# Optimization experiments

Measured on AMD Instinct MI355X. Metric: run time of the kernel, lower is better.

Reference implementation:

```python
import jax, jax.numpy as jnp
import numpy as np

EPS = 1e-12


def agnn_layer(x, row, col, num_nodes):
    """AGNN propagation with beta frozen at 1.0 (requires_grad=False in source).
    alpha_ij = softmax_{j in N(i)} ( beta * cos(x_i, x_j) ); out_i = sum_j alpha_ij * x_j.
    row = destination node of each edge (segment id), col = source node.
    """
    xn = x / (jnp.linalg.norm(x, axis=-1, keepdims=True) + EPS)  # unit-norm features
    score = jnp.sum(xn[row] * xn[col], axis=-1)                   # [E] beta=1 * cos sim
    smax = jax.ops.segment_max(score, row, num_segments=num_nodes)
    e = jnp.exp(score - smax[row])                                # stable softmax numerator
    denom = jax.ops.segment_sum(e, row, num_segments=num_nodes)
    alpha = e / jnp.maximum(denom[row], EPS)                      # [E]
    out = jax.ops.segment_sum(alpha[:, None] * x[col], row, num_segments=num_nodes)
    return out


def setup_inputs() -> dict:
    key = jax.random.key(0)
    ks = jax.random.split(key, 8)
    N, E = 100000, 1600000
    IN_DIM, HID, OUT_DIM = 128, 64, 64
    x = jax.random.normal(ks[0], (N, IN_DIM), dtype=jnp.float32)
    edge_row = jnp.sort(jax.random.randint(ks[1], (E,), 0, N))
    edge_col = jax.random.randint(ks[2], (E,), 0, N)
    # Linear params (PyTorch nn.Linear style: y = x @ W.T + b)
    s1 = 1.0 / np.sqrt(IN_DIM)
    W1 = jax.random.uniform(ks[3], (HID, IN_DIM), jnp.float32, -s1, s1)
    b1 = jax.random.uniform(ks[4], (HID,), jnp.float32, -s1, s1)
    s2 = 1.0 / np.sqrt(HID)
    W2 = jax.random.uniform(ks[5], (OUT_DIM, HID), jnp.float32, -s2, s2)
    b2 = jax.random.uniform(ks[6], (OUT_DIM,), jnp.float32, -s2, s2)
    return {"x": x, "edge_row": edge_row, "edge_col": edge_col,
            "W1": W1, "b1": b1, "W2": W2, "b2": b2}


def reference(x, edge_row, edge_col, W1, b1, W2, b2):
    N = x.shape[0]
    h = jax.nn.relu(x @ W1.T + b1)
    for _ in range(4):  # 4 frozen-beta AGNN layers
        h = jax.nn.relu(agnn_layer(h, edge_row, edge_col, N))
    return h @ W2.T + b2
```

## Files before the change

kernel.cpp:

```cpp
#include <hip/hip_runtime.h>


typedef _Float16 h2 __attribute__((ext_vector_type(2)));

union U4H { uint4 u; h2 h[4]; };
union U2H { uint2 u; h2 h[2]; };
union UHI { unsigned u; h2 h; };
union UF  { unsigned u; float f; int i; };

#define DEV_INLINE __device__ __forceinline__

DEV_INLINE h2 mkh2(float a, float b) {
    h2 r; r.x = (_Float16)a; r.y = (_Float16)b; return r;
}

template <int CTRL>
DEV_INLINE float dpp_addf(float x) {
    UF a, b;
    a.f = x;
    b.i = __builtin_amdgcn_update_dpp(0, a.i, CTRL, 0xF, 0xF, true);
    return x + b.f;
}

__global__ __launch_bounds__(256) void build_rowptr_scan(const int* __restrict__ row,
                                                         int* __restrict__ ptr,
                                                         int N, int E) {
    int e = blockIdx.x * blockDim.x + threadIdx.x;
    if (e >= E) return;
    const int r1 = row[e];
    const int r0 = (e == 0) ? -1 : row[e - 1];
    for (int i = r0 + 1; i <= r1; ++i) ptr[i] = e;
    if (e == E - 1) {
        for (int i = r1 + 1; i <= N; ++i) ptr[i] = E;
    }
}

#define PSEG 1024
__global__ __launch_bounds__(1024) void build_perm_seg(const int* __restrict__ ptr,
                                                       int4* __restrict__ meta,
                                                       int N) {
    __shared__ int hist[256];
    __shared__ int tmp[256];
    const int t    = threadIdx.x;
    const int base = blockIdx.x * PSEG;
    const int end  = (base + PSEG < N) ? base + PSEG : N;
    const int cnt  = end - base;

    if (t < 256) hist[t] = 0;
    __syncthreads();

    int d = -1, p0v = 0, p1v = 0;
    if (t < cnt) {
        p0v = ptr[base + t];
        p1v = ptr[base + t + 1];
        d = p1v - p0v;
        if (d > 255) d = 255;
        atomicAdd(&hist[d], 1);
    }
    __syncthreads();

    int h0 = (t < 256) ? hist[t] : 0;
    int* src = hist; int* dst = tmp;
    for (int off = 1; off < 256; off <<= 1) {
        if (t < 256) dst[t] = src[t] + (t >= off ? src[t - off] : 0);
        __syncthreads();
        int* tt = src; src = dst; dst = tt;
    }
    if (t < 256) src[t] -= h0;
    __syncthreads();

    if (t < cnt) {
        int pos = base + atomicAdd(&src[d], 1);
        meta[pos] = make_int4(base + t, p0v, p1v, 0);
    }
}

__global__ __launch_bounds__(512) void gemm1_relu(const float* __restrict__ x,
                                                  const float* __restrict__ W1,
                                                  const float* __restrict__ b1,
                                                  unsigned short* __restrict__ xn,
                                                  float* __restrict__ nrm,
                                                  int N) {
    __shared__ __align__(16) float Wt[32 * 64];
    __shared__ __align__(16) float xT[32 * 128];
    const int tid  = threadIdx.x;
    const int tx   = tid & 15;
    const int ty   = tid >> 4;
    const int base = blockIdx.x * 128;

    const float4* W4  = (const float4*)W1;
    const float4* x4p = (const float4*)x;

    const int wO  = tid & 63;
    const int wK4 = tid >> 6;
    const int mA  = tid & 127;
    const int kA  = tid >> 7;
    const int mB  = mA;
    const int kB  = kA + 4;
    const int nodeA = base + mA;

    float4 wv, xa_, xb_;
    wv = W4[wO * 32 + wK4];
    xa_ = make_float4(0.f, 0.f, 0.f, 0.f);
    xb_ = xa_;
    if (nodeA < N) {
        xa_ = x4p[(size_t)nodeA * 32 + kA];
        xb_ = x4p[(size_t)nodeA * 32 + kB];
    }

    float4 b4 = ((const float4*)b1)[tx];
    float4 acc[4];
    acc[0] = b4; acc[1] = b4; acc[2] = b4; acc[3] = b4;

    for (int c = 0; c < 4; ++c) {
        Wt[(4 * wK4 + 0) * 64 + wO] = wv.x;
        Wt[(4 * wK4 + 1) * 64 + wO] = wv.y;
        Wt[(4 * wK4 + 2) * 64 + wO] = wv.z;
        Wt[(4 * wK4 + 3) * 64 + wO] = wv.w;
        xT[(4 * kA + 0) * 128 + mA] = xa_.x;
        xT[(4 * kA + 1) * 128 + mA] = xa_.y;
        xT[(4 * kA + 2) * 128 + mA] = xa_.z;
        xT[(4 * kA + 3) * 128 + mA] = xa_.w;
        xT[(4 * kB + 0) * 128 + mB] = xb_.x;
        xT[(4 * kB + 1) * 128 + mB] = xb_.y;
        xT[(4 * kB + 2) * 128 + mB] = xb_.z;
        xT[(4 * kB + 3) * 128 + mB] = xb_.w;
        __syncthreads();

        if (c < 3) {
            const int ko = (c + 1) * 8;
            wv = W4[wO * 32 + ko + wK4];
            if (nodeA < N) {
                xa_ = x4p[(size_t)nodeA * 32 + ko + kA];
                xb_ = x4p[(size_t)nodeA * 32 + ko + kB];
            }
        }

#pragma unroll 4
        for (int k = 0; k < 32; ++k) {
            const float4 w4 = *(const float4*)&Wt[k * 64 + 4 * tx];
            const float4 xv = *(const float4*)&xT[k * 128 + 4 * ty];
            acc[0].x = fmaf(xv.x, w4.x, acc[0].x);
            acc[0].y = fmaf(xv.x, w4.y, acc[0].y);
            acc[0].z = fmaf(xv.x, w4.z, acc[0].z);
            acc[0].w = fmaf(xv.x, w4.w, acc[0].w);
            acc[1].x = fmaf(xv.y, w4.x, acc[1].x);
            acc[1].y = fmaf(xv.y, w4.y, acc[1].y);
            acc[1].z = fmaf(xv.y, w4.z, acc[1].z);
            acc[1].w = fmaf(xv.y, w4.w, acc[1].w);
            acc[2].x = fmaf(xv.z, w4.x, acc[2].x);
            acc[2].y = fmaf(xv.z, w4.y, acc[2].y);
            acc[2].z = fmaf(xv.z, w4.z, acc[2].z);
            acc[2].w = fmaf(xv.z, w4.w, acc[2].w);
            acc[3].x = fmaf(xv.w, w4.x, acc[3].x);
            acc[3].y = fmaf(xv.w, w4.y, acc[3].y);
            acc[3].z = fmaf(xv.w, w4.z, acc[3].z);
            acc[3].w = fmaf(xv.w, w4.w, acc[3].w);
        }
        if (c < 3) __syncthreads();
    }

#pragma unroll
    for (int mm = 0; mm < 4; ++mm) {
        float4 r = acc[mm];
        r.x = fmaxf(r.x, 0.f); r.y = fmaxf(r.y, 0.f);
        r.z = fmaxf(r.z, 0.f); r.w = fmaxf(r.w, 0.f);
        float s = fmaf(r.x, r.x, fmaf(r.y, r.y, fmaf(r.z, r.z, r.w * r.w)));
        s = dpp_addf<0xB1>(s);
        s = dpp_addf<0x4E>(s);
        s = dpp_addf<0x141>(s);
        s = dpp_addf<0x140>(s);
        const float nn  = sqrtf(s) + 1e-12f;
        const float inv = 1.f / nn;
        int node = base + 4 * ty + mm;
        if (node < N) {
            U2H pk;
            pk.h[0] = mkh2(r.x * inv, r.y * inv);
            pk.h[1] = mkh2(r.z * inv, r.w * inv);
            *(uint2*)&xn[(size_t)node * 64 + 4 * tx] = pk.u;
            if (tx == mm) nrm[node] = nn;
        }
    }
}

__global__ __launch_bounds__(256, 6) void agnn_layer(const uint4* __restrict__ xn4,
                                                     const float* __restrict__ nrm,
                                                     const int4* __restrict__ meta,
                                                     const int* __restrict__ col,
                                                     uint4* __restrict__ xo4,
                                                     float* __restrict__ nrmo,
                                                     int N) {
    const int tid  = threadIdx.x;
    const int lane = tid & 63;
    const int g    = (lane >> 3) & 1;
    const int sub  = lane & 7;
    const int slot = blockIdx.x * 16 + (tid >> 4);
    if (slot >= N) return;

    const int4 m0 = meta[slot];
    const int i  = m0.x;
    const int p0 = m0.y, p1 = m0.z;

    U4H hi_;
    hi_.u = xn4[(unsigned)i * 8u + sub];
    {
        const _Float16 L2E = (_Float16)1.4426950408889634f;
        h2 l2 = {L2E, L2E};
#pragma unroll
        for (int c = 0; c < 4; ++c) hi_.h[c] *= l2;
    }

    const int mid = p0 + ((p1 - p0 + 1) >> 1);
    int       t   = g ? mid : p0;
    const int e_  = g ? p1  : mid;

    float den = 0.f;
    U4H acc;
    acc.h[0] = mkh2(0.f, 0.f); acc.h[1] = mkh2(0.f, 0.f);
    acc.h[2] = mkh2(0.f, 0.f); acc.h[3] = mkh2(0.f, 0.f);

    for (; t < e_; t += 8) {
        const int nb = e_ - t;
        int   jj[8];
        uint4 v[8];
        float nm[8];

#pragma unroll
        for (int k = 0; k < 8; ++k) {
            int e = t + k;
            e = (e < e_) ? e : (e_ - 1);
            jj[k] = col[e];
        }
#pragma unroll
        for (int k = 0; k < 8; ++k) v[k] = xn4[(unsigned)jj[k] * 8u + sub];
#pragma unroll
        for (int k = 0; k < 8; ++k) nm[k] = nrm[jj[k]];

#pragma unroll
        for (int k = 0; k < 8; ++k) {
            U4H xa; xa.u = v[k];
            float sa = __builtin_amdgcn_fdot2(hi_.h[0], xa.h[0], 0.f, false);
            sa = __builtin_amdgcn_fdot2(hi_.h[1], xa.h[1], sa, false);
            float sb = __builtin_amdgcn_fdot2(hi_.h[2], xa.h[2], 0.f, false);
            sb = __builtin_amdgcn_fdot2(hi_.h[3], xa.h[3], sb, false);
            float s = sa + sb;
            s = dpp_addf<0xB1>(s);
            s = dpp_addf<0x4E>(s);
            s = dpp_addf<0x141>(s);
            const float p = (k < nb) ? exp2f(s) : 0.f;
            den += p;
            const _Float16 wh = (_Float16)(p * nm[k]);
            h2 w2 = {wh, wh};
            acc.h[0] += w2 * xa.h[0];
            acc.h[1] += w2 * xa.h[1];
            acc.h[2] += w2 * xa.h[2];
            acc.h[3] += w2 * xa.h[3];
        }
    }

    den = dpp_addf<0x140>(den);
#pragma unroll
    for (int c = 0; c < 4; ++c) {
        UHI a; a.h = acc.h[c];
        UHI b; b.u = (unsigned)__shfl_xor((int)a.u, 8, 64);
        acc.h[c] = a.h + b.h;
    }

    const float id = 1.f / fmaxf(den, 1e-12f);
    float o[8];
#pragma unroll
    for (int c = 0; c < 4; ++c) {
        o[2 * c]     = fmaxf((float)acc.h[c].x * id, 0.f);
        o[2 * c + 1] = fmaxf((float)acc.h[c].y * id, 0.f);
    }

    float s2 = 0.f;
#pragma unroll
    for (int c = 0; c < 8; ++c) s2 = fmaf(o[c], o[c], s2);
    s2 = dpp_addf<0xB1>(s2);
    s2 = dpp_addf<0x4E>(s2);
    s2 = dpp_addf<0x141>(s2);
    const float nn  = sqrtf(s2) + 1e-12f;
    const float inv = 1.f / nn;

    if (g == 0) {
        U4H ov;
        ov.h[0] = mkh2(o[0] * inv, o[1] * inv);
        ov.h[1] = mkh2(o[2] * inv, o[3] * inv);
        ov.h[2] = mkh2(o[4] * inv, o[5] * inv);
        ov.h[3] = mkh2(o[6] * inv, o[7] * inv);
        xo4[(unsigned)i * 8u + sub] = ov.u;
        if (sub == 0) nrmo[i] = nn;
    }
}

__global__ __launch_bounds__(512) void gemm2(const unsigned short* __restrict__ xn,
                                             const float* __restrict__ nrm,
                                             const float* __restrict__ W2,
                                             const float* __restrict__ b2,
                                             float* __restrict__ out,
                                             int N) {
    __shared__ __align__(16) float Wt[64 * 64];
    __shared__ __align__(16) float xT[64 * 128];
    const int tid  = threadIdx.x;
    const int tx   = tid & 15;
    const int ty   = tid >> 4;
    const int base = blockIdx.x * 128;

    {
        const float4* W4 = (const float4*)W2;
#pragma unroll
        for (int it = 0; it < 2; ++it) {
            int idx = tid + it * 512;
            int o = idx & 63, k4 = idx >> 6;
            float4 v = W4[o * 16 + k4];
            Wt[(4 * k4 + 0) * 64 + o] = v.x;
            Wt[(4 * k4 + 1) * 64 + o] = v.y;
            Wt[(4 * k4 + 2) * 64 + o] = v.z;
            Wt[(4 * k4 + 3) * 64 + o] = v.w;
        }
        const uint2* x2 = (const uint2*)xn;
#pragma unroll
        for (int it = 0; it < 4; ++it) {
            int idx = tid + it * 512;
            int mm = idx & 127, k4 = idx >> 7;
            int node = base + mm;
            U2H v; v.u = make_uint2(0u, 0u);
            float nn = 0.f;
            if (node < N) { v.u = x2[(size_t)node * 16 + k4]; nn = nrm[node]; }
            xT[(4 * k4 + 0) * 128 + mm] = (float)v.h[0].x * nn;
            xT[(4 * k4 + 1) * 128 + mm] = (float)v.h[0].y * nn;
            xT[(4 * k4 + 2) * 128 + mm] = (float)v.h[1].x * nn;
            xT[(4 * k4 + 3) * 128 + mm] = (float)v.h[1].y * nn;
        }
    }
    __syncthreads();

    float4 b4 = ((const float4*)b2)[tx];
    float4 acc[4];
    acc[0] = b4; acc[1] = b4; acc[2] = b4; acc[3] = b4;

#pragma unroll 4
    for (int k = 0; k < 64; ++k) {
        const float4 w4 = *(const float4*)&Wt[k * 64 + 4 * tx];
        const float4 xv = *(const float4*)&xT[k * 128 + 4 * ty];
        acc[0].x = fmaf(xv.x, w4.x, acc[0].x);
        acc[0].y = fmaf(xv.x, w4.y, acc[0].y);
        acc[0].z = fmaf(xv.x, w4.z, acc[0].z);
        acc[0].w = fmaf(xv.x, w4.w, acc[0].w);
        acc[1].x = fmaf(xv.y, w4.x, acc[1].x);
        acc[1].y = fmaf(xv.y, w4.y, acc[1].y);
        acc[1].z = fmaf(xv.y, w4.z, acc[1].z);
        acc[1].w = fmaf(xv.y, w4.w, acc[1].w);
        acc[2].x = fmaf(xv.z, w4.x, acc[2].x);
        acc[2].y = fmaf(xv.z, w4.y, acc[2].y);
        acc[2].z = fmaf(xv.z, w4.z, acc[2].z);
        acc[2].w = fmaf(xv.z, w4.w, acc[2].w);
        acc[3].x = fmaf(xv.w, w4.x, acc[3].x);
        acc[3].y = fmaf(xv.w, w4.y, acc[3].y);
        acc[3].z = fmaf(xv.w, w4.z, acc[3].z);
        acc[3].w = fmaf(xv.w, w4.w, acc[3].w);
    }

#pragma unroll
    for (int mm = 0; mm < 4; ++mm) {
        int node = base + 4 * ty + mm;
        if (node < N) *(float4*)&out[(size_t)node * 64 + 4 * tx] = acc[mm];
    }
}

extern "C" void kernel_launch(void* const* d_in, const int* in_sizes, int n_in,
                              void* d_out, int out_size, void* d_ws, size_t ws_size,
                              hipStream_t stream) {
    const float* x   = (const float*)d_in[0];
    const int*   row = (const int*)d_in[1];
    const int*   col = (const int*)d_in[2];
    const float* W1  = (const float*)d_in[3];
    const float* b1  = (const float*)d_in[4];
    const float* W2  = (const float*)d_in[5];
    const float* b2  = (const float*)d_in[6];
    float* out = (float*)d_out;

    const int N = in_sizes[0] / 128;
    const int E = in_sizes[1];

    char* ws = (char*)d_ws;
    size_t off = 0;
    unsigned short* ha = (unsigned short*)(ws + off); off += (size_t)N * 64 * 2;
    unsigned short* hb = (unsigned short*)(ws + off); off += (size_t)N * 64 * 2;
    float* na_  = (float*)(ws + off); off += (size_t)N * sizeof(float);
    float* nb_  = (float*)(ws + off); off += (size_t)N * sizeof(float);
    int*   ptr  = (int*)  (ws + off); off += (size_t)(N + 1) * sizeof(int);
    off = (off + 15) & ~(size_t)15;
    int4*  meta = (int4*) (ws + off); off += (size_t)N * sizeof(int4);
    (void)ws_size; (void)n_in; (void)out_size;

    build_rowptr_scan<<<(E + 255) / 256, 256, 0, stream>>>(row, ptr, N, E);

    build_perm_seg<<<(N + PSEG - 1) / PSEG, 1024, 0, stream>>>(ptr, meta, N);

    const int nbG = (N + 127) / 128;
    gemm1_relu<<<nbG, 512, 0, stream>>>(x, W1, b1, ha, na_, N);

    const int nb16 = (N + 15) / 16;
    unsigned short* hc = ha; unsigned short* hn = hb;
    float* nc = na_; float* nn = nb_;
    for (int l = 0; l < 4; ++l) {
        agnn_layer<<<nb16, 256, 0, stream>>>((const uint4*)hc, nc, meta, col,
                                             (uint4*)hn, nn, N);
        unsigned short* t = hc; hc = hn; hn = t;
        float* tf = nc; nc = nn; nn = tf;
    }

    gemm2<<<nbG, 512, 0, stream>>>(hc, nc, W2, b2, out, N);
}
```

Baseline: 296.7 us.

## Double rows per thread in both dense GEMMs and pipeline gemm2 K-chunks

```diff
diff --git a/kernel.cpp b/kernel.cpp
--- a/kernel.cpp
+++ b/kernel.cpp
@@ -75,6 +75,40 @@
     }
 }
 
+#define GEMM_BODY(w4, xa, xb)                                   \
+    acc[0].x = fmaf(xa.x, w4.x, acc[0].x);                      \
+    acc[0].y = fmaf(xa.x, w4.y, acc[0].y);                      \
+    acc[0].z = fmaf(xa.x, w4.z, acc[0].z);                      \
+    acc[0].w = fmaf(xa.x, w4.w, acc[0].w);                      \
+    acc[1].x = fmaf(xa.y, w4.x, acc[1].x);                      \
+    acc[1].y = fmaf(xa.y, w4.y, acc[1].y);                      \
+    acc[1].z = fmaf(xa.y, w4.z, acc[1].z);                      \
+    acc[1].w = fmaf(xa.y, w4.w, acc[1].w);                      \
+    acc[2].x = fmaf(xa.z, w4.x, acc[2].x);                      \
+    acc[2].y = fmaf(xa.z, w4.y, acc[2].y);                      \
+    acc[2].z = fmaf(xa.z, w4.z, acc[2].z);                      \
+    acc[2].w = fmaf(xa.z, w4.w, acc[2].w);                      \
+    acc[3].x = fmaf(xa.w, w4.x, acc[3].x);                      \
+    acc[3].y = fmaf(xa.w, w4.y, acc[3].y);                      \
+    acc[3].z = fmaf(xa.w, w4.z, acc[3].z);                      \
+    acc[3].w = fmaf(xa.w, w4.w, acc[3].w);                      \
+    acc[4].x = fmaf(xb.x, w4.x, acc[4].x);                      \
+    acc[4].y = fmaf(xb.x, w4.y, acc[4].y);                      \
+    acc[4].z = fmaf(xb.x, w4.z, acc[4].z);                      \
+    acc[4].w = fmaf(xb.x, w4.w, acc[4].w);                      \
+    acc[5].x = fmaf(xb.y, w4.x, acc[5].x);                      \
+    acc[5].y = fmaf(xb.y, w4.y, acc[5].y);                      \
+    acc[5].z = fmaf(xb.y, w4.z, acc[5].z);                      \
+    acc[5].w = fmaf(xb.y, w4.w, acc[5].w);                      \
+    acc[6].x = fmaf(xb.z, w4.x, acc[6].x);                      \
+    acc[6].y = fmaf(xb.z, w4.y, acc[6].y);                      \
+    acc[6].z = fmaf(xb.z, w4.z, acc[6].z);                      \
+    acc[6].w = fmaf(xb.z, w4.w, acc[6].w);                      \
+    acc[7].x = fmaf(xb.w, w4.x, acc[7].x);                      \
+    acc[7].y = fmaf(xb.w, w4.y, acc[7].y);                      \
+    acc[7].z = fmaf(xb.w, w4.z, acc[7].z);                      \
+    acc[7].w = fmaf(xb.w, w4.w, acc[7].w);
+
 __global__ __launch_bounds__(512) void gemm1_relu(const float* __restrict__ x,
                                                   const float* __restrict__ W1,
                                                   const float* __restrict__ b1,
@@ -82,86 +116,70 @@
                                                   float* __restrict__ nrm,
                                                   int N) {
     __shared__ __align__(16) float Wt[32 * 64];
-    __shared__ __align__(16) float xT[32 * 128];
+    __shared__ __align__(16) float xT[32 * 256];
     const int tid  = threadIdx.x;
     const int tx   = tid & 15;
     const int ty   = tid >> 4;
-    const int base = blockIdx.x * 128;
+    const int base = blockIdx.x * 256;
 
     const float4* W4  = (const float4*)W1;
     const float4* x4p = (const float4*)x;
 
     const int wO  = tid & 63;
     const int wK4 = tid >> 6;
-    const int mA  = tid & 127;
-    const int kA  = tid >> 7;
-    const int mB  = mA;
-    const int kB  = kA + 4;
+    const int mA  = tid & 255;
+    const int kb  = tid >> 8;
     const int nodeA = base + mA;
-
-    float4 wv, xa_, xb_;
+    const bool okA  = nodeA < N;
+
+    float4 wv, xv[4];
     wv = W4[wO * 32 + wK4];
-    xa_ = make_float4(0.f, 0.f, 0.f, 0.f);
-    xb_ = xa_;
-    if (nodeA < N) {
-        xa_ = x4p[(size_t)nodeA * 32 + kA];
-        xb_ = x4p[(size_t)nodeA * 32 + kB];
+#pragma unroll
+    for (int it = 0; it < 4; ++it) {
+        xv[it] = make_float4(0.f, 0.f, 0.f, 0.f);
+        if (okA) xv[it] = x4p[(size_t)nodeA * 32 + kb + 2 * it];
     }
 
     float4 b4 = ((const float4*)b1)[tx];
-    float4 acc[4];
-    acc[0] = b4; acc[1] = b4; acc[2] = b4; acc[3] = b4;
+    float4 acc[8];
+#pragma unroll
+    for (int mm = 0; mm < 8; ++mm) acc[mm] = b4;
 
     for (int c = 0; c < 4; ++c) {
         Wt[(4 * wK4 + 0) * 64 + wO] = wv.x;
         Wt[(4 * wK4 + 1) * 64 + wO] = wv.y;
         Wt[(4 * wK4 + 2) * 64 + wO] = wv.z;
         Wt[(4 * wK4 + 3) * 64 + wO] = wv.w;
-        xT[(4 * kA + 0) * 128 + mA] = xa_.x;
-        xT[(4 * kA + 1) * 128 + mA] = xa_.y;
-        xT[(4 * kA + 2) * 128 + mA] = xa_.z;
-        xT[(4 * kA + 3) * 128 + mA] = xa_.w;
-        xT[(4 * kB + 0) * 128 + mB] = xb_.x;
-        xT[(4 * kB + 1) * 128 + mB] = xb_.y;
-        xT[(4 * kB + 2) * 128 + mB] = xb_.z;
-        xT[(4 * kB + 3) * 128 + mB] = xb_.w;
+#pragma unroll
+        for (int it = 0; it < 4; ++it) {
+            const int k4 = kb + 2 * it;
+            xT[(4 * k4 + 0) * 256 + mA] = xv[it].x;
+            xT[(4 * k4 + 1) * 256 + mA] = xv[it].y;
+            xT[(4 * k4 + 2) * 256 + mA] = xv[it].z;
+            xT[(4 * k4 + 3) * 256 + mA] = xv[it].w;
+        }
         __syncthreads();
 
         if (c < 3) {
             const int ko = (c + 1) * 8;
             wv = W4[wO * 32 + ko + wK4];
-            if (nodeA < N) {
-                xa_ = x4p[(size_t)nodeA * 32 + ko + kA];
-                xb_ = x4p[(size_t)nodeA * 32 + ko + kB];
-            }
+#pragma unroll
+            for (int it = 0; it < 4; ++it)
+                if (okA) xv[it] = x4p[(size_t)nodeA * 32 + ko + kb + 2 * it];
         }
 
 #pragma unroll 4
         for (int k = 0; k < 32; ++k) {
             const float4 w4 = *(const float4*)&Wt[k * 64 + 4 * tx];
-            const float4 xv = *(const float4*)&xT[k * 128 + 4 * ty];
-            acc[0].x = fmaf(xv.x, w4.x, acc[0].x);
-            acc[0].y = fmaf(xv.x, w4.y, acc[0].y);
-            acc[0].z = fmaf(xv.x, w4.z, acc[0].z);
-            acc[0].w = fmaf(xv.x, w4.w, acc[0].w);
-            acc[1].x = fmaf(xv.y, w4.x, acc[1].x);
-            acc[1].y = fmaf(xv.y, w4.y, acc[1].y);
-            acc[1].z = fmaf(xv.y, w4.z, acc[1].z);
-            acc[1].w = fmaf(xv.y, w4.w, acc[1].w);
-            acc[2].x = fmaf(xv.z, w4.x, acc[2].x);
-            acc[2].y = fmaf(xv.z, w4.y, acc[2].y);
-            acc[2].z = fmaf(xv.z, w4.z, acc[2].z);
-            acc[2].w = fmaf(xv.z, w4.w, acc[2].w);
-            acc[3].x = fmaf(xv.w, w4.x, acc[3].x);
-            acc[3].y = fmaf(xv.w, w4.y, acc[3].y);
-            acc[3].z = fmaf(xv.w, w4.z, acc[3].z);
-            acc[3].w = fmaf(xv.w, w4.w, acc[3].w);
+            const float4 xa = *(const float4*)&xT[k * 256 + 8 * ty];
+            const float4 xb = *(const float4*)&xT[k * 256 + 8 * ty + 4];
+            GEMM_BODY(w4, xa, xb)
         }
         if (c < 3) __syncthreads();
     }
 
 #pragma unroll
-    for (int mm = 0; mm < 4; ++mm) {
+    for (int mm = 0; mm < 8; ++mm) {
         float4 r = acc[mm];
         r.x = fmaxf(r.x, 0.f); r.y = fmaxf(r.y, 0.f);
         r.z = fmaxf(r.z, 0.f); r.w = fmaxf(r.w, 0.f);
@@ -172,7 +190,7 @@
         s = dpp_addf<0x140>(s);
         const float nn  = sqrtf(s) + 1e-12f;
         const float inv = 1.f / nn;
-        int node = base + 4 * ty + mm;
+        int node = base + 8 * ty + mm;
         if (node < N) {
             U2H pk;
             pk.h[0] = mkh2(r.x * inv, r.y * inv);
@@ -300,71 +318,75 @@
                                              const float* __restrict__ b2,
                                              float* __restrict__ out,
                                              int N) {
-    __shared__ __align__(16) float Wt[64 * 64];
-    __shared__ __align__(16) float xT[64 * 128];
+    __shared__ __align__(16) float Wt[32 * 64];
+    __shared__ __align__(16) float xT[32 * 256];
     const int tid  = threadIdx.x;
     const int tx   = tid & 15;
     const int ty   = tid >> 4;
-    const int base = blockIdx.x * 128;
-
-    {
-        const float4* W4 = (const float4*)W2;
-#pragma unroll
-        for (int it = 0; it < 2; ++it) {
-            int idx = tid + it * 512;
-            int o = idx & 63, k4 = idx >> 6;
-            float4 v = W4[o * 16 + k4];
-            Wt[(4 * k4 + 0) * 64 + o] = v.x;
-            Wt[(4 * k4 + 1) * 64 + o] = v.y;
-            Wt[(4 * k4 + 2) * 64 + o] = v.z;
-            Wt[(4 * k4 + 3) * 64 + o] = v.w;
-        }
-        const uint2* x2 = (const uint2*)xn;
+    const int base = blockIdx.x * 256;
+
+    const float4* W4 = (const float4*)W2;
+    const uint2*  x2 = (const uint2*)xn;
+
+    const int wO  = tid & 63;
+    const int wK4 = tid >> 6;
+    const int mA  = tid & 255;
+    const int kb  = tid >> 8;
+    const int nodeA = base + mA;
+    const bool okA  = nodeA < N;
+
+    float nnA = 0.f;
+    if (okA) nnA = nrm[nodeA];
+
+    float4 wv;
+    U2H xv[4];
+    wv = W4[wO * 16 + wK4];
+#pragma unroll
+    for (int it = 0; it < 4; ++it) {
+        xv[it].u = make_uint2(0u, 0u);
+        if (okA) xv[it].u = x2[(size_t)nodeA * 16 + kb + 2 * it];
+    }
+
+    float4 b4 = ((const float4*)b2)[tx];
+    float4 acc[8];
+#pragma unroll
+    for (int mm = 0; mm < 8; ++mm) acc[mm] = b4;
+
+    for (int c = 0; c < 2; ++c) {
+        Wt[(4 * wK4 + 0) * 64 + wO] = wv.x;
+        Wt[(4 * wK4 + 1) * 64 + wO] = wv.y;
+        Wt[(4 * wK4 + 2) * 64 + wO] = wv.z;
+        Wt[(4 * wK4 + 3) * 64 + wO] = wv.w;
 #pragma unroll
         for (int it = 0; it < 4; ++it) {
-            int idx = tid + it * 512;
-            int mm = idx & 127, k4 = idx >> 7;
-            int node = base + mm;
-            U2H v; v.u = make_uint2(0u, 0u);
-            float nn = 0.f;
-            if (node < N) { v.u = x2[(size_t)node * 16 + k4]; nn = nrm[node]; }
-            xT[(4 * k4 + 0) * 128 + mm] = (float)v.h[0].x * nn;
-            xT[(4 * k4 + 1) * 128 + mm] = (float)v.h[0].y * nn;
-            xT[(4 * k4 + 2) * 128 + mm] = (float)v.h[1].x * nn;
-            xT[(4 * k4 + 3) * 128 + mm] = (float)v.h[1].y * nn;
-        }
-    }
-    __syncthreads();
-
-    float4 b4 = ((const float4*)b2)[tx];
-    float4 acc[4];
-    acc[0] = b4; acc[1] = b4; acc[2] = b4; acc[3] = b4;
+            const int k4 = kb + 2 * it;
+            xT[(4 * k4 + 0) * 256 + mA] = (float)xv[it].h[0].x * nnA;
+            xT[(4 * k4 + 1) * 256 + mA] = (float)xv[it].h[0].y * nnA;
+            xT[(4 * k4 + 2) * 256 + mA] = (float)xv[it].h[1].x * nnA;
+            xT[(4 * k4 + 3) * 256 + mA] = (float)xv[it].h[1].y * nnA;
+        }
+        __syncthreads();
+
+        if (c == 0) {
+            wv = W4[wO * 16 + 8 + wK4];
+#pragma unroll
+            for (int it = 0; it < 4; ++it)
+                if (okA) xv[it].u = x2[(size_t)nodeA * 16 + 8 + kb + 2 * it];
+        }
 
 #pragma unroll 4
-    for (int k = 0; k < 64; ++k) {
-        const float4 w4 = *(const float4*)&Wt[k * 64 + 4 * tx];
-        const float4 xv = *(const float4*)&xT[k * 128 + 4 * ty];
-        acc[0].x = fmaf(xv.x, w4.x, acc[0].x);
-        acc[0].y = fmaf(xv.x, w4.y, acc[0].y);
-        acc[0].z = fmaf(xv.x, w4.z, acc[0].z);
-        acc[0].w = fmaf(xv.x, w4.w, acc[0].w);
-        acc[1].x = fmaf(xv.y, w4.x, acc[1].x);
-        acc[1].y = fmaf(xv.y, w4.y, acc[1].y);
-        acc[1].z = fmaf(xv.y, w4.z, acc[1].z);
-        acc[1].w = fmaf(xv.y, w4.w, acc[1].w);
-        acc[2].x = fmaf(xv.z, w4.x, acc[2].x);
-        acc[2].y = fmaf(xv.z, w4.y, acc[2].y);
-        acc[2].z = fmaf(xv.z, w4.z, acc[2].z);
-        acc[2].w = fmaf(xv.z, w4.w, acc[2].w);
-        acc[3].x = fmaf(xv.w, w4.x, acc[3].x);
-        acc[3].y = fmaf(xv.w, w4.y, acc[3].y);
-        acc[3].z = fmaf(xv.w, w4.z, acc[3].z);
-        acc[3].w = fmaf(xv.w, w4.w, acc[3].w);
-    }
-
-#pragma unroll
-    for (int mm = 0; mm < 4; ++mm) {
-        int node = base + 4 * ty + mm;
+        for (int k = 0; k < 32; ++k) {
+            const float4 w4 = *(const float4*)&Wt[k * 64 + 4 * tx];
+            const float4 xa = *(const float4*)&xT[k * 256 + 8 * ty];
+            const float4 xb = *(const float4*)&xT[k * 256 + 8 * ty + 4];
+            GEMM_BODY(w4, xa, xb)
+        }
+        if (c == 0) __syncthreads();
+    }
+
+#pragma unroll
+    for (int mm = 0; mm < 8; ++mm) {
+        int node = base + 8 * ty + mm;
         if (node < N) *(float4*)&out[(size_t)node * 64 + 4 * tx] = acc[mm];
     }
 }
@@ -399,7 +421,7 @@
 
     build_perm_seg<<<(N + PSEG - 1) / PSEG, 1024, 0, stream>>>(ptr, meta, N);
 
-    const int nbG = (N + 127) / 128;
+    const int nbG = (N + 255) / 256;
     gemm1_relu<<<nbG, 512, 0, stream>>>(x, W1, b1, ha, na_, N);
 
     const int nb16 = (N + 15) / 16;
```

Result: no change. 299.2 us (+0.8%).
